# Optimization experiments

Hardware: AMD Instinct MI355X
Metric: run time of the kernel (lower is better)

## Reference

```python
import jax, jax.numpy as jnp
import numpy as np

B, T, D, H = 4, 2048, 1024, 16
S = D // H  # head dim

def setup_inputs() -> dict:
    key = jax.random.key(0)
    kx, kq, ku, kb = jax.random.split(key, 4)
    x = jax.random.normal(kx, (B, T, D), dtype=jnp.float32)
    # torch nn.Linear weights: (out, in); y = x @ W.T
    Wq = jax.random.normal(kq, (D, D), dtype=jnp.float32) * (1.0 / np.sqrt(D))
    Wu = jax.random.normal(ku, (D, D), dtype=jnp.float32) * (1.0 / np.sqrt(D))
    bu = jax.random.normal(kb, (D,), dtype=jnp.float32) * 0.01
    return {"x": x, "Wq": Wq, "Wu": Wu, "bu": bu}

def reference(x, Wq, Wu, bu):
    b, t, k = x.shape
    h, s = H, S
    # Bug in original module replicated: Q, K, V all use to_queries.
    q = x @ Wq.T  # (b,t,k)
    qh = q.reshape(b, t, h, s).transpose(0, 2, 1, 3)  # (b,h,t,s)
    scores = jnp.einsum('bhts,bhus->bhtu', qh, qh) / jnp.sqrt(jnp.asarray(s, x.dtype))
    w = jax.nn.softmax(scores, axis=-1)  # (b,h,t,t)
    out = jnp.einsum('bhtu,bhus->bhts', w, qh)  # (b,h,t,s)
    out = out.transpose(0, 2, 1, 3).reshape(b, t, k)  # merge heads
    return out @ Wu.T + bu
```

## Files before the change

### kernel.cpp

```cpp
#include <hip/hip_runtime.h>

#define B_ 4
#define T_ 2048
#define D_ 1024
#define H_ 16
#define S_ 64

typedef __attribute__((ext_vector_type(8))) short bf16x8;
typedef __attribute__((ext_vector_type(16))) float f32x16;
typedef unsigned int uint;

__device__ __forceinline__ short f2bf(float f) {
    union { float f; uint u; } v; v.f = f;
    uint r = v.u + 0x7fffu + ((v.u >> 16) & 1u);
    return (short)(r >> 16);
}

__device__ __forceinline__ void gld16(const short* g, short* l) {
    __builtin_amdgcn_global_load_lds((const __attribute__((address_space(1))) void*)g,
                                     (__attribute__((address_space(3))) void*)l, 16, 0, 0);
}

__global__ __launch_bounds__(256) void cvt3(const float* __restrict__ x,
                                            const float* __restrict__ wq,
                                            const float* __restrict__ wu,
                                            short* __restrict__ xb,
                                            short* __restrict__ wqb,
                                            short* __restrict__ wub) {
    const int NX = B_ * T_ * D_ / 8;
    const int NW = D_ * D_ / 8;
    int i = blockIdx.x * 256 + threadIdx.x;
    const float* src; short* dst; int off;
    if (i < NX)            { src = x;  dst = xb;  off = i; }
    else if (i < NX + NW)  { src = wq; dst = wqb; off = i - NX; }
    else                   { src = wu; dst = wub; off = i - NX - NW; }
    float4 a = *(const float4*)(src + (size_t)off * 8);
    float4 b = *(const float4*)(src + (size_t)off * 8 + 4);
    short o[8] = {f2bf(a.x), f2bf(a.y), f2bf(a.z), f2bf(a.w),
                  f2bf(b.x), f2bf(b.y), f2bf(b.z), f2bf(b.w)};
    *(bf16x8*)(dst + (size_t)off * 8) = *(bf16x8*)o;
}

template <bool OUT_BF16>
__global__ __launch_bounds__(256, 2) void gemm_bt(const short* __restrict__ A,
                                                  const short* __restrict__ Bt,
                                                  const float* __restrict__ bias,
                                                  void* __restrict__ Cv,
                                                  int M, int N, int K) {
    __shared__ short As[4096];
    __shared__ short Bs[4096];
    const int tid  = threadIdx.x;
    const int lane = tid & 63;
    const int wv   = tid >> 6;
    const int wm   = wv >> 1, wn = wv & 1;
    const int h32  = lane >> 5;
    const int m0 = blockIdx.y * 128, n0 = blockIdx.x * 128;
    const short* Ap = A + (size_t)m0 * K;
    const short* Bp = Bt + (size_t)n0 * K;

    f32x16 acc[2][2];
    #pragma unroll
    for (int i = 0; i < 2; ++i)
        #pragma unroll
        for (int j = 0; j < 2; ++j)
            #pragma unroll
            for (int r = 0; r < 16; ++r) acc[i][j][r] = 0.f;

    for (int k0 = 0; k0 < K; k0 += 32) {
        __syncthreads();
        gld16(Ap + (size_t)lane * K        + k0 + wv * 8, &As[(wv * 128) * 8]);
        gld16(Ap + (size_t)(64 + lane) * K + k0 + wv * 8, &As[(wv * 128 + 64) * 8]);
        gld16(Bp + (size_t)lane * K        + k0 + wv * 8, &Bs[(wv * 128) * 8]);
        gld16(Bp + (size_t)(64 + lane) * K + k0 + wv * 8, &Bs[(wv * 128 + 64) * 8]);
        __syncthreads();

        #pragma unroll
        for (int ks2 = 0; ks2 < 2; ++ks2) {
            const int kk8 = ks2 * 2 + h32;
            bf16x8 af[2], bfr[2];
            af[0]  = *(bf16x8*)&As[(kk8 * 128 + wm * 64 + (lane & 31)) * 8];
            af[1]  = *(bf16x8*)&As[(kk8 * 128 + wm * 64 + 32 + (lane & 31)) * 8];
            bfr[0] = *(bf16x8*)&Bs[(kk8 * 128 + wn * 64 + (lane & 31)) * 8];
            bfr[1] = *(bf16x8*)&Bs[(kk8 * 128 + wn * 64 + 32 + (lane & 31)) * 8];
            acc[0][0] = __builtin_amdgcn_mfma_f32_32x32x16_bf16(af[0], bfr[0], acc[0][0], 0, 0, 0);
            acc[0][1] = __builtin_amdgcn_mfma_f32_32x32x16_bf16(af[0], bfr[1], acc[0][1], 0, 0, 0);
            acc[1][0] = __builtin_amdgcn_mfma_f32_32x32x16_bf16(af[1], bfr[0], acc[1][0], 0, 0, 0);
            acc[1][1] = __builtin_amdgcn_mfma_f32_32x32x16_bf16(af[1], bfr[1], acc[1][1], 0, 0, 0);
        }
    }

    #pragma unroll
    for (int mt = 0; mt < 2; ++mt) {
        #pragma unroll
        for (int nt = 0; nt < 2; ++nt) {
            const int rbase = m0 + wm * 64 + mt * 32;
            const int col   = n0 + wn * 64 + nt * 32 + (lane & 31);
            float bv = 0.f;
            if (!OUT_BF16 && bias) bv = bias[col];
            #pragma unroll
            for (int r = 0; r < 16; ++r) {
                int row = rbase + (r & 3) + 8 * (r >> 2) + 4 * h32;
                if constexpr (OUT_BF16)
                    ((short*)Cv)[(size_t)row * N + col] = f2bf(acc[mt][nt][r]);
                else
                    ((float*)Cv)[(size_t)row * N + col] = acc[mt][nt][r] + bv;
            }
        }
    }
}

__global__ __launch_bounds__(256, 2) void attn_mfma(const short* __restrict__ q,
                                                    short* __restrict__ o) {
    __shared__ short smem[8192];
    const int tid  = threadIdx.x;
    const int lane = tid & 63;
    const int wv   = tid >> 6;
    const int h32  = lane >> 5;
    const int b  = blockIdx.y >> 4;
    const int hh = blockIdx.y & 15;
    const int t0 = blockIdx.x * 128;
    const short* qb = q + (size_t)b * (T_ * D_) + hh * S_;

    #pragma unroll
    for (int rep = 0; rep < 4; ++rep) {
        int f = rep * 256 + tid;
        int r = f >> 3, c8 = f & 7;
        bf16x8 v = *(const bf16x8*)(qb + (size_t)(t0 + r) * D_ + c8 * 8);
        *(bf16x8*)&smem[(c8 * 128 + (r ^ c8)) * 8] = v;
    }
    __syncthreads();
    bf16x8 Qreg[4];
    #pragma unroll
    for (int ks = 0; ks < 4; ++ks) {
        int kk8 = 2 * ks + h32;
        Qreg[ks] = *(bf16x8*)&smem[(kk8 * 128 + ((wv * 32 + (lane & 31)) ^ kk8)) * 8];
    }

    f32x16 accO0, accO1;
    #pragma unroll
    for (int i = 0; i < 16; ++i) { accO0[i] = 0.f; accO1[i] = 0.f; }
    float lsp = 0.f;
    const int prow16 = ((((lane & 7) << 2) | ((lane >> 3) & 3)) * 16) + h32 * 512;

    for (int u0 = 0; u0 < T_; u0 += 64) {
        __syncthreads();
        #pragma unroll
        for (int rep = 0; rep < 2; ++rep) {
            int f = rep * 256 + tid;
            int uu = f >> 3, c8 = f & 7;
            int u = (uu & 0x33) | ((uu & 4) << 1) | ((uu & 8) >> 1);
            bf16x8 v = *(const bf16x8*)(qb + (size_t)(u0 + u) * D_ + c8 * 8);
            *(bf16x8*)&smem[(c8 * 64 + (u ^ c8)) * 8] = v;
            short sv[8];
            *(bf16x8*)sv = v;
            int base = 4096 + (u >> 4) * 1024 + ((u >> 2) & 1) * 512 + (c8 >> 2) * 8
                     + ((u & 3) | (((u >> 3) & 1) << 2)) + (c8 & 3) * 16;
            #pragma unroll
            for (int ds = 0; ds < 8; ++ds)
                smem[base + ds * 64] = sv[ds];
        }
        __syncthreads();

        f32x16 aS0, aS1;
        #pragma unroll
        for (int i = 0; i < 16; ++i) { aS0[i] = 0.f; aS1[i] = 0.f; }
        #pragma unroll
        for (int ks = 0; ks < 4; ++ks) {
            int kk8 = 2 * ks + h32;
            bf16x8 k0 = *(bf16x8*)&smem[(kk8 * 64 + ((lane & 31) ^ kk8)) * 8];
            bf16x8 k1 = *(bf16x8*)&smem[(kk8 * 64 + ((32 + (lane & 31)) ^ kk8)) * 8];
            aS0 = __builtin_amdgcn_mfma_f32_32x32x16_bf16(k0, Qreg[ks], aS0, 0, 0, 0);
            aS1 = __builtin_amdgcn_mfma_f32_32x32x16_bf16(k1, Qreg[ks], aS1, 0, 0, 0);
        }

        bf16x8 af[4];
        #pragma unroll
        for (int tt = 0; tt < 2; ++tt) {
            const f32x16& a = tt ? aS1 : aS0;
            float p[16];
            #pragma unroll
            for (int r = 0; r < 16; ++r) { p[r] = __expf(a[r] * 0.125f); lsp += p[r]; }
            #pragma unroll
            for (int sub = 0; sub < 2; ++sub) {
                union { uint u[4]; bf16x8 v; } cv;
                #pragma unroll
                for (int dd = 0; dd < 4; ++dd)
                    cv.u[dd] = __builtin_amdgcn_perm(
                        __float_as_uint(p[sub * 8 + 2 * dd + 1]),
                        __float_as_uint(p[sub * 8 + 2 * dd]), 0x07060302u);
                af[tt * 2 + sub] = cv.v;
            }
        }

        #pragma unroll
        for (int c = 0; c < 4; ++c) {
            bf16x8 v0 = *(bf16x8*)&smem[4096 + c * 1024 + prow16 + 0];
            bf16x8 v1 = *(bf16x8*)&smem[4096 + c * 1024 + prow16 + 8];
            accO0 = __builtin_amdgcn_mfma_f32_32x32x16_bf16(af[c], v0, accO0, 0, 0, 0);
            accO1 = __builtin_amdgcn_mfma_f32_32x32x16_bf16(af[c], v1, accO1, 0, 0, 0);
        }
    }

    float dsum = lsp + __shfl_xor(lsp, 32);
    short* ob = o + (size_t)b * (T_ * D_) + hh * S_;
    #pragma unroll
    for (int r = 0; r < 16; ++r) {
        int rt = (r & 3) + 8 * (r >> 2) + 4 * h32;
        float inv = 1.00390625f / __shfl(dsum, rt);
        size_t t = (size_t)(t0 + wv * 32 + rt);
        ob[t * D_ + (lane & 31)]      = f2bf(accO0[r] * inv);
        ob[t * D_ + 32 + (lane & 31)] = f2bf(accO1[r] * inv);
    }
}

extern "C" void kernel_launch(void* const* d_in, const int* in_sizes, int n_in,
                              void* d_out, int out_size, void* d_ws, size_t ws_size,
                              hipStream_t stream) {
    const float* x  = (const float*)d_in[0];
    const float* Wq = (const float*)d_in[1];
    const float* Wu = (const float*)d_in[2];
    const float* bu = (const float*)d_in[3];
    float* out  = (float*)d_out;
    short* qbuf = (short*)d_out;
    short* xb   = (short*)((char*)d_out + 16777216);
    short* attn = (short*)d_ws;
    short* wqb  = (short*)((char*)d_ws + 16777216);
    short* wub  = (short*)((char*)d_ws + 18874368);

    const int M = B_ * T_;
    dim3 blk(256);
    dim3 gg(D_ / 128, M / 128);
    hipLaunchKernelGGL(cvt3, dim3(5120), blk, 0, stream, x, Wq, Wu, xb, wqb, wub);
    hipLaunchKernelGGL((gemm_bt<true>), gg, blk, 0, stream,
                       xb, wqb, (const float*)nullptr, (void*)qbuf, M, D_, D_);
    hipLaunchKernelGGL(attn_mfma, dim3(T_ / 128, B_ * H_), blk, 0, stream, qbuf, attn);
    hipLaunchKernelGGL((gemm_bt<false>), gg, blk, 0, stream,
                       attn, wub, bu, (void*)out, M, D_, D_);
}
```

Measured before the change: 258.4 us.

## Double-buffer GEMM, pre-transpose Q, and restructure attention to load K/V into registers

The projection GEMM now double-buffers its LDS tiles so the next K-slice load overlaps the current MFMAs, with one barrier per iteration. A new transpose kernel writes a per-head transposed copy of Q so the attention kernel can read V fragments straight from global memory. Attention drops LDS staging, processes 256 query rows per block (two 32-row groups per wave), and uses exp2 with the scale sqrt(1/8·log2 e) folded into the Q projection output, correcting with a constant in the final normalisation. This removes shared-memory staging and barriers but adds a transpose pass, heavier register use, and uncoalesced, redundant global loads of K/V per wave.

```diff
diff --git a/kernel.cpp b/kernel.cpp
--- a/kernel.cpp
+++ b/kernel.cpp
@@ -41,14 +41,46 @@
     *(bf16x8*)(dst + (size_t)off * 8) = *(bf16x8*)o;
 }
 
+__global__ __launch_bounds__(256) void transp(const short* __restrict__ q,
+                                              short* __restrict__ qT) {
+    __shared__ short L[64 * 68];
+    const int tid = threadIdx.x;
+    const int bh = blockIdx.y;
+    const int t0 = blockIdx.x * 64;
+    const short* qh = q + (size_t)(bh >> 4) * (T_ * D_) + (bh & 15) * S_;
+    #pragma unroll
+    for (int rep = 0; rep < 2; ++rep) {
+        int f = rep * 256 + tid;
+        int r = f >> 3, c8 = f & 7;
+        bf16x8 v = *(const bf16x8*)(qh + (size_t)(t0 + r) * D_ + c8 * 8);
+        short sv[8]; *(bf16x8*)sv = v;
+        #pragma unroll
+        for (int ds = 0; ds < 8; ++ds)
+            L[(c8 * 8 + ds) * 68 + r] = sv[ds];
+    }
+    __syncthreads();
+    #pragma unroll
+    for (int rep = 0; rep < 2; ++rep) {
+        int f = rep * 256 + tid;
+        int s = f >> 3, pc = f & 7;
+        int bt = (pc >> 1) * 16 + (pc & 1) * 4;
+        short o[8];
+        #pragma unroll
+        for (int j = 0; j < 4; ++j) o[j]     = L[s * 68 + bt + j];
+        #pragma unroll
+        for (int j = 0; j < 4; ++j) o[4 + j] = L[s * 68 + bt + 8 + j];
+        *(bf16x8*)(qT + ((size_t)bh * S_ + s) * T_ + t0 + pc * 8) = *(bf16x8*)o;
+    }
+}
+
 template <bool OUT_BF16>
 __global__ __launch_bounds__(256, 2) void gemm_bt(const short* __restrict__ A,
                                                   const short* __restrict__ Bt,
                                                   const float* __restrict__ bias,
                                                   void* __restrict__ Cv,
-                                                  int M, int N, int K) {
-    __shared__ short As[4096];
-    __shared__ short Bs[4096];
+                                                  int M, int N, int K, float oscale) {
+    __shared__ short As[2][4096];
+    __shared__ short Bs[2][4096];
     const int tid  = threadIdx.x;
     const int lane = tid & 63;
     const int wv   = tid >> 6;
@@ -66,27 +98,36 @@
             #pragma unroll
             for (int r = 0; r < 16; ++r) acc[i][j][r] = 0.f;
 
+    gld16(Ap + (size_t)lane * K        + wv * 8, &As[0][(wv * 128) * 8]);
+    gld16(Ap + (size_t)(64 + lane) * K + wv * 8, &As[0][(wv * 128 + 64) * 8]);
+    gld16(Bp + (size_t)lane * K        + wv * 8, &Bs[0][(wv * 128) * 8]);
+    gld16(Bp + (size_t)(64 + lane) * K + wv * 8, &Bs[0][(wv * 128 + 64) * 8]);
+    __syncthreads();
+
+    int p = 0;
     for (int k0 = 0; k0 < K; k0 += 32) {
-        __syncthreads();
-        gld16(Ap + (size_t)lane * K        + k0 + wv * 8, &As[(wv * 128) * 8]);
-        gld16(Ap + (size_t)(64 + lane) * K + k0 + wv * 8, &As[(wv * 128 + 64) * 8]);
-        gld16(Bp + (size_t)lane * K        + k0 + wv * 8, &Bs[(wv * 128) * 8]);
-        gld16(Bp + (size_t)(64 + lane) * K + k0 + wv * 8, &Bs[(wv * 128 + 64) * 8]);
-        __syncthreads();
-
+        if (k0 + 32 < K) {
+            int kn = k0 + 32;
+            gld16(Ap + (size_t)lane * K        + kn + wv * 8, &As[1 - p][(wv * 128) * 8]);
+            gld16(Ap + (size_t)(64 + lane) * K + kn + wv * 8, &As[1 - p][(wv * 128 + 64) * 8]);
+            gld16(Bp + (size_t)lane * K        + kn + wv * 8, &Bs[1 - p][(wv * 128) * 8]);
+            gld16(Bp + (size_t)(64 + lane) * K + kn + wv * 8, &Bs[1 - p][(wv * 128 + 64) * 8]);
+        }
         #pragma unroll
         for (int ks2 = 0; ks2 < 2; ++ks2) {
             const int kk8 = ks2 * 2 + h32;
             bf16x8 af[2], bfr[2];
-            af[0]  = *(bf16x8*)&As[(kk8 * 128 + wm * 64 + (lane & 31)) * 8];
-            af[1]  = *(bf16x8*)&As[(kk8 * 128 + wm * 64 + 32 + (lane & 31)) * 8];
-            bfr[0] = *(bf16x8*)&Bs[(kk8 * 128 + wn * 64 + (lane & 31)) * 8];
-            bfr[1] = *(bf16x8*)&Bs[(kk8 * 128 + wn * 64 + 32 + (lane & 31)) * 8];
+            af[0]  = *(bf16x8*)&As[p][(kk8 * 128 + wm * 64 + (lane & 31)) * 8];
+            af[1]  = *(bf16x8*)&As[p][(kk8 * 128 + wm * 64 + 32 + (lane & 31)) * 8];
+            bfr[0] = *(bf16x8*)&Bs[p][(kk8 * 128 + wn * 64 + (lane & 31)) * 8];
+            bfr[1] = *(bf16x8*)&Bs[p][(kk8 * 128 + wn * 64 + 32 + (lane & 31)) * 8];
             acc[0][0] = __builtin_amdgcn_mfma_f32_32x32x16_bf16(af[0], bfr[0], acc[0][0], 0, 0, 0);
             acc[0][1] = __builtin_amdgcn_mfma_f32_32x32x16_bf16(af[0], bfr[1], acc[0][1], 0, 0, 0);
             acc[1][0] = __builtin_amdgcn_mfma_f32_32x32x16_bf16(af[1], bfr[0], acc[1][0], 0, 0, 0);
             acc[1][1] = __builtin_amdgcn_mfma_f32_32x32x16_bf16(af[1], bfr[1], acc[1][1], 0, 0, 0);
         }
+        __syncthreads();
+        p ^= 1;
     }
 
     #pragma unroll
@@ -101,7 +142,7 @@
             for (int r = 0; r < 16; ++r) {
                 int row = rbase + (r & 3) + 8 * (r >> 2) + 4 * h32;
                 if constexpr (OUT_BF16)
-                    ((short*)Cv)[(size_t)row * N + col] = f2bf(acc[mt][nt][r]);
+                    ((short*)Cv)[(size_t)row * N + col] = f2bf(acc[mt][nt][r] * oscale);
                 else
                     ((float*)Cv)[(size_t)row * N + col] = acc[mt][nt][r] + bv;
             }
@@ -110,106 +151,106 @@
 }
 
 __global__ __launch_bounds__(256, 2) void attn_mfma(const short* __restrict__ q,
+                                                    const short* __restrict__ qT,
                                                     short* __restrict__ o) {
-    __shared__ short smem[8192];
     const int tid  = threadIdx.x;
     const int lane = tid & 63;
     const int wv   = tid >> 6;
     const int h32  = lane >> 5;
-    const int b  = blockIdx.y >> 4;
-    const int hh = blockIdx.y & 15;
-    const int t0 = blockIdx.x * 128;
-    const short* qb = q + (size_t)b * (T_ * D_) + hh * S_;
-
-    #pragma unroll
-    for (int rep = 0; rep < 4; ++rep) {
-        int f = rep * 256 + tid;
-        int r = f >> 3, c8 = f & 7;
-        bf16x8 v = *(const bf16x8*)(qb + (size_t)(t0 + r) * D_ + c8 * 8);
-        *(bf16x8*)&smem[(c8 * 128 + (r ^ c8)) * 8] = v;
-    }
-    __syncthreads();
-    bf16x8 Qreg[4];
-    #pragma unroll
-    for (int ks = 0; ks < 4; ++ks) {
-        int kk8 = 2 * ks + h32;
-        Qreg[ks] = *(bf16x8*)&smem[(kk8 * 128 + ((wv * 32 + (lane & 31)) ^ kk8)) * 8];
-    }
-
-    f32x16 accO0, accO1;
-    #pragma unroll
-    for (int i = 0; i < 16; ++i) { accO0[i] = 0.f; accO1[i] = 0.f; }
-    float lsp = 0.f;
-    const int prow16 = ((((lane & 7) << 2) | ((lane >> 3) & 3)) * 16) + h32 * 512;
-
+    const int l31  = lane & 31;
+    const int bh = blockIdx.y;
+    const int b  = bh >> 4, hh = bh & 15;
+    const int t0 = blockIdx.x * 256;
+    const short* qh = q + (size_t)b * (T_ * D_) + hh * S_;
+    const short* qr = qT + (size_t)bh * S_ * T_;
+
+    bf16x8 Qreg[2][4];
+    #pragma unroll
+    for (int g = 0; g < 2; ++g) {
+        int tq = t0 + wv * 64 + g * 32 + l31;
+        #pragma unroll
+        for (int ks = 0; ks < 4; ++ks)
+            Qreg[g][ks] = *(const bf16x8*)(qh + (size_t)tq * D_ + (2 * ks + h32) * 8);
+    }
+
+    f32x16 accO[2][2];
+    #pragma unroll
+    for (int g = 0; g < 2; ++g)
+        #pragma unroll
+        for (int s = 0; s < 2; ++s)
+            #pragma unroll
+            for (int r = 0; r < 16; ++r) accO[g][s][r] = 0.f;
+    float lsa[2] = {0.f, 0.f}, lsb[2] = {0.f, 0.f};
+
+    #pragma unroll 1
     for (int u0 = 0; u0 < T_; u0 += 64) {
-        __syncthreads();
-        #pragma unroll
-        for (int rep = 0; rep < 2; ++rep) {
-            int f = rep * 256 + tid;
-            int uu = f >> 3, c8 = f & 7;
-            int u = (uu & 0x33) | ((uu & 4) << 1) | ((uu & 8) >> 1);
-            bf16x8 v = *(const bf16x8*)(qb + (size_t)(u0 + u) * D_ + c8 * 8);
-            *(bf16x8*)&smem[(c8 * 64 + (u ^ c8)) * 8] = v;
-            short sv[8];
-            *(bf16x8*)sv = v;
-            int base = 4096 + (u >> 4) * 1024 + ((u >> 2) & 1) * 512 + (c8 >> 2) * 8
-                     + ((u & 3) | (((u >> 3) & 1) << 2)) + (c8 & 3) * 16;
-            #pragma unroll
-            for (int ds = 0; ds < 8; ++ds)
-                smem[base + ds * 64] = sv[ds];
-        }
-        __syncthreads();
-
-        f32x16 aS0, aS1;
-        #pragma unroll
-        for (int i = 0; i < 16; ++i) { aS0[i] = 0.f; aS1[i] = 0.f; }
-        #pragma unroll
-        for (int ks = 0; ks < 4; ++ks) {
-            int kk8 = 2 * ks + h32;
-            bf16x8 k0 = *(bf16x8*)&smem[(kk8 * 64 + ((lane & 31) ^ kk8)) * 8];
-            bf16x8 k1 = *(bf16x8*)&smem[(kk8 * 64 + ((32 + (lane & 31)) ^ kk8)) * 8];
-            aS0 = __builtin_amdgcn_mfma_f32_32x32x16_bf16(k0, Qreg[ks], aS0, 0, 0, 0);
-            aS1 = __builtin_amdgcn_mfma_f32_32x32x16_bf16(k1, Qreg[ks], aS1, 0, 0, 0);
-        }
-
-        bf16x8 af[4];
-        #pragma unroll
-        for (int tt = 0; tt < 2; ++tt) {
-            const f32x16& a = tt ? aS1 : aS0;
-            float p[16];
-            #pragma unroll
-            for (int r = 0; r < 16; ++r) { p[r] = __expf(a[r] * 0.125f); lsp += p[r]; }
-            #pragma unroll
-            for (int sub = 0; sub < 2; ++sub) {
-                union { uint u[4]; bf16x8 v; } cv;
+        bf16x8 Kf[2][4], Vf[4][2];
+        #pragma unroll
+        for (int kh = 0; kh < 2; ++kh) {
+            int u = u0 + kh * 32 + l31;
+            #pragma unroll
+            for (int ks = 0; ks < 4; ++ks)
+                Kf[kh][ks] = *(const bf16x8*)(qh + (size_t)u * D_ + (2 * ks + h32) * 8);
+        }
+        #pragma unroll
+        for (int c = 0; c < 4; ++c)
+            #pragma unroll
+            for (int sh = 0; sh < 2; ++sh)
+                Vf[c][sh] = *(const bf16x8*)(qr + (size_t)(sh * 32 + l31) * T_
+                                             + u0 + c * 16 + h32 * 8);
+
+        #pragma unroll
+        for (int g = 0; g < 2; ++g) {
+            f32x16 aS0, aS1;
+            #pragma unroll
+            for (int i = 0; i < 16; ++i) { aS0[i] = 0.f; aS1[i] = 0.f; }
+            #pragma unroll
+            for (int ks = 0; ks < 4; ++ks) {
+                aS0 = __builtin_amdgcn_mfma_f32_32x32x16_bf16(Kf[0][ks], Qreg[g][ks], aS0, 0, 0, 0);
+                aS1 = __builtin_amdgcn_mfma_f32_32x32x16_bf16(Kf[1][ks], Qreg[g][ks], aS1, 0, 0, 0);
+            }
+            bf16x8 af[4];
+            #pragma unroll
+            for (int kh = 0; kh < 2; ++kh) {
+                const f32x16& a = kh ? aS1 : aS0;
+                float p[16];
                 #pragma unroll
-                for (int dd = 0; dd < 4; ++dd)
-                    cv.u[dd] = __builtin_amdgcn_perm(
-                        __float_as_uint(p[sub * 8 + 2 * dd + 1]),
-                        __float_as_uint(p[sub * 8 + 2 * dd]), 0x07060302u);
-                af[tt * 2 + sub] = cv.v;
-            }
-        }
-
-        #pragma unroll
-        for (int c = 0; c < 4; ++c) {
-            bf16x8 v0 = *(bf16x8*)&smem[4096 + c * 1024 + prow16 + 0];
-            bf16x8 v1 = *(bf16x8*)&smem[4096 + c * 1024 + prow16 + 8];
-            accO0 = __builtin_amdgcn_mfma_f32_32x32x16_bf16(af[c], v0, accO0, 0, 0, 0);
-            accO1 = __builtin_amdgcn_mfma_f32_32x32x16_bf16(af[c], v1, accO1, 0, 0, 0);
-        }
-    }
-
-    float dsum = lsp + __shfl_xor(lsp, 32);
+                for (int r = 0; r < 16; ++r) {
+                    p[r] = __builtin_amdgcn_exp2f(a[r]);
+                    if (r & 1) lsb[g] += p[r]; else lsa[g] += p[r];
+                }
+                #pragma unroll
+                for (int sub = 0; sub < 2; ++sub) {
+                    union { uint u[4]; bf16x8 v; } cv;
+                    #pragma unroll
+                    for (int dd = 0; dd < 4; ++dd)
+                        cv.u[dd] = __builtin_amdgcn_perm(
+                            __float_as_uint(p[sub * 8 + 2 * dd + 1]),
+                            __float_as_uint(p[sub * 8 + 2 * dd]), 0x07060302u);
+                    af[kh * 2 + sub] = cv.v;
+                }
+            }
+            #pragma unroll
+            for (int c = 0; c < 4; ++c) {
+                accO[g][0] = __builtin_amdgcn_mfma_f32_32x32x16_bf16(af[c], Vf[c][0], accO[g][0], 0, 0, 0);
+                accO[g][1] = __builtin_amdgcn_mfma_f32_32x32x16_bf16(af[c], Vf[c][1], accO[g][1], 0, 0, 0);
+            }
+        }
+    }
+
     short* ob = o + (size_t)b * (T_ * D_) + hh * S_;
     #pragma unroll
-    for (int r = 0; r < 16; ++r) {
-        int rt = (r & 3) + 8 * (r >> 2) + 4 * h32;
-        float inv = 1.00390625f / __shfl(dsum, rt);
-        size_t t = (size_t)(t0 + wv * 32 + rt);
-        ob[t * D_ + (lane & 31)]      = f2bf(accO0[r] * inv);
-        ob[t * D_ + 32 + (lane & 31)] = f2bf(accO1[r] * inv);
+    for (int g = 0; g < 2; ++g) {
+        float ds = lsa[g] + lsb[g];
+        ds += __shfl_xor(ds, 32);
+        #pragma unroll
+        for (int r = 0; r < 16; ++r) {
+            int rt = (r & 3) + 8 * (r >> 2) + 4 * h32;
+            float inv = 2.3594089f / __shfl(ds, rt);
+            size_t t = (size_t)(t0 + wv * 64 + g * 32 + rt);
+            ob[t * D_ + l31]      = f2bf(accO[g][0][r] * inv);
+            ob[t * D_ + 32 + l31] = f2bf(accO[g][1][r] * inv);
+        }
     }
 }
 
@@ -223,6 +264,7 @@
     float* out  = (float*)d_out;
     short* qbuf = (short*)d_out;
     short* xb   = (short*)((char*)d_out + 16777216);
+    short* qT   = xb;
     short* attn = (short*)d_ws;
     short* wqb  = (short*)((char*)d_ws + 16777216);
     short* wub  = (short*)((char*)d_ws + 18874368);
@@ -232,8 +274,9 @@
     dim3 gg(D_ / 128, M / 128);
     hipLaunchKernelGGL(cvt3, dim3(5120), blk, 0, stream, x, Wq, Wu, xb, wqb, wub);
     hipLaunchKernelGGL((gemm_bt<true>), gg, blk, 0, stream,
-                       xb, wqb, (const float*)nullptr, (void*)qbuf, M, D_, D_);
-    hipLaunchKernelGGL(attn_mfma, dim3(T_ / 128, B_ * H_), blk, 0, stream, qbuf, attn);
+                       xb, wqb, (const float*)nullptr, (void*)qbuf, M, D_, D_, 0.42466090f);
+    hipLaunchKernelGGL(transp, dim3(T_ / 64, B_ * H_), blk, 0, stream, qbuf, qT);
+    hipLaunchKernelGGL(attn_mfma, dim3(T_ / 256, B_ * H_), blk, 0, stream, qbuf, qT, attn);
     hipLaunchKernelGGL((gemm_bt<false>), gg, blk, 0, stream,
-                       attn, wub, bu, (void*)out, M, D_, D_);
-}
+                       attn, wub, bu, (void*)out, M, D_, D_, 1.0f);
+}
```

Result: slower. 299.6 us (+15.9%).
